# Kernel tuning notes

Hardware: AMD Instinct MI355X
Metric: run time of the kernel (lower is better)

The kernel has to match this reference:

```python
import jax, jax.numpy as jnp
import numpy as np
from jax.ops import segment_sum, segment_max

N_NODES = 50000
N_EDGES = 800000
N_GRAPHS = 512


def setup_inputs() -> dict:
    key = jax.random.key(0)
    ks = jax.random.split(key, 12)
    s = 0.1
    x = jax.random.normal(ks[0], (N_NODES, 3), dtype=jnp.float32)
    edge_index = jax.random.randint(ks[1], (2, N_EDGES), 0, N_NODES, dtype=jnp.int64)
    batch = jnp.sort(jax.random.randint(ks[2], (N_NODES,), 0, N_GRAPHS, dtype=jnp.int64))
    # GATConv(3, 64, heads=4): W [3, 4*64], att [4,64] each
    W1 = jax.random.normal(ks[3], (3, 256), dtype=jnp.float32) * s
    att_src1 = jax.random.normal(ks[4], (4, 64), dtype=jnp.float32) * s
    att_dst1 = jax.random.normal(ks[5], (4, 64), dtype=jnp.float32) * s
    bias1 = jnp.zeros((256,), dtype=jnp.float32)
    # GATConv(256, 128, heads=1)
    W2 = jax.random.normal(ks[6], (256, 128), dtype=jnp.float32) * s
    att_src2 = jax.random.normal(ks[7], (1, 128), dtype=jnp.float32) * s
    att_dst2 = jax.random.normal(ks[8], (1, 128), dtype=jnp.float32) * s
    bias2 = jnp.zeros((128,), dtype=jnp.float32)
    # Linear(128, 2)
    fcW = jax.random.normal(ks[9], (128, 2), dtype=jnp.float32) * s
    fcb = jnp.zeros((2,), dtype=jnp.float32)
    return {"x": x, "edge_index": edge_index, "batch": batch,
            "W1": W1, "att_src1": att_src1, "att_dst1": att_dst1, "bias1": bias1,
            "W2": W2, "att_src2": att_src2, "att_dst2": att_dst2, "bias2": bias2,
            "fcW": fcW, "fcb": fcb}


def gat_conv(x, src, dst, W, att_src, att_dst, bias):
    """PyG-style GATConv (concat heads). src->dst messages, softmax over dst."""
    N = x.shape[0]
    H, C = att_src.shape
    h = (x @ W).reshape(N, H, C)                      # [N,H,C]
    a_src = jnp.einsum('nhc,hc->nh', h, att_src)      # [N,H]
    a_dst = jnp.einsum('nhc,hc->nh', h, att_dst)      # [N,H]
    e = jax.nn.leaky_relu(a_src[src] + a_dst[dst], 0.2)  # [E,H]
    # segment softmax over incoming edges of each dst node
    emax = segment_max(e, dst, num_segments=N)        # [N,H]
    ee = jnp.exp(e - emax[dst])
    denom = segment_sum(ee, dst, num_segments=N)      # [N,H]
    alpha = ee / (denom[dst] + 1e-16)                 # [E,H]
    out = segment_sum(alpha[:, :, None] * h[src], dst, num_segments=N)  # [N,H,C]
    return out.reshape(N, H * C) + bias


def reference(x, edge_index, batch, W1, att_src1, att_dst1, bias1,
              W2, att_src2, att_dst2, bias2, fcW, fcb):
    N = x.shape[0]
    loops = jnp.arange(N, dtype=edge_index.dtype)
    src = jnp.concatenate([edge_index[0], loops])     # add self-loops (PyG default)
    dst = jnp.concatenate([edge_index[1], loops])
    h = jax.nn.relu(gat_conv(x, src, dst, W1, att_src1, att_dst1, bias1))
    h = jax.nn.relu(gat_conv(h, src, dst, W2, att_src2, att_dst2, bias2))
    # global mean pool per graph
    sums = segment_sum(h, batch, num_segments=N_GRAPHS)                # [G,128]
    counts = segment_sum(jnp.ones((N, 1), h.dtype), batch, num_segments=N_GRAPHS)
    pooled = sums / jnp.maximum(counts, 1.0)
    return pooled @ fcW + fcb                          # [G,2]
```

## Files before the change

### kernel.cpp

```cpp
#include <hip/hip_runtime.h>
#include <hip/hip_bf16.h>

#define NN 50000
#define NE 800000
#define NG 512
#define NCHUNK 196
#define NROWPAD 50048
#define CAP 64

#define NBUK 196
#define BCAP 5120
#define BSTRIDE 16
#define LBCAP 32

#define SCAT_BLKS 782
#define A1P_BLKS 196
#define W2B_BLKS 128
#define BND_BLKS 3
#define FRONT_GRID (SCAT_BLKS + A1P_BLKS + W2B_BLKS + BND_BLKS)

typedef __attribute__((ext_vector_type(8))) short bf16x8;
typedef __attribute__((ext_vector_type(4))) float f32x4;

static __device__ __forceinline__ float lrelu(float x) { return x > 0.f ? x : 0.2f * x; }

static __device__ __forceinline__ ushort f2b(float f) {
    __hip_bfloat16 b = __float2bfloat16(f);
    return *(ushort*)&b;
}
static __device__ __forceinline__ float b2f(ushort u) {
    union { unsigned int i; float f; } v; v.i = ((unsigned int)u) << 16; return v.f;
}

__global__ __launch_bounds__(256) void k_front(
        const int* __restrict__ ei, int* __restrict__ bcnt, unsigned int* __restrict__ bstore,
        const float* __restrict__ x, const float* __restrict__ W1,
        const float* __restrict__ attS1, const float* __restrict__ attD1,
        float* __restrict__ xa1, float* __restrict__ a1d,
        const float* __restrict__ W2, ushort* __restrict__ wtb,
        const int* __restrict__ batch, int* __restrict__ bounds) {
    int b = blockIdx.x, tid = threadIdx.x;
    if (b < SCAT_BLKS) {
        __shared__ unsigned int lrec[LBCAP * NBUK];
        __shared__ int lcnt[NBUK];
        for (int i = tid; i < NBUK; i += 256) lcnt[i] = 0;
        __syncthreads();
        int t = b * 256 + tid;
        int base4 = t * 4;
        if (base4 < NE) {
            int4 sv = *(const int4*)(ei + base4);
            int4 dv = *(const int4*)(ei + NE + base4);
            int d, s, bin, p;
            d = dv.x; s = sv.x; bin = d >> 8;
            p = atomicAdd(&lcnt[bin], 1);
            lrec[p * NBUK + bin] = ((unsigned int)s << 8) | (unsigned int)(d & 255);
            d = dv.y; s = sv.y; bin = d >> 8;
            p = atomicAdd(&lcnt[bin], 1);
            lrec[p * NBUK + bin] = ((unsigned int)s << 8) | (unsigned int)(d & 255);
            d = dv.z; s = sv.z; bin = d >> 8;
            p = atomicAdd(&lcnt[bin], 1);
            lrec[p * NBUK + bin] = ((unsigned int)s << 8) | (unsigned int)(d & 255);
            d = dv.w; s = sv.w; bin = d >> 8;
            p = atomicAdd(&lcnt[bin], 1);
            lrec[p * NBUK + bin] = ((unsigned int)s << 8) | (unsigned int)(d & 255);
        }
        __syncthreads();
        if (tid < NBUK) {
            int c = lcnt[tid];
            if (c) {
                int base = atomicAdd(&bcnt[tid * BSTRIDE], c);
                unsigned int* dst = bstore + (size_t)tid * BCAP + base;
                for (int q = 0; q < c; q++) dst[q] = lrec[q * NBUK + tid];
            }
        }
    } else if (b < SCAT_BLKS + A1P_BLKS) {
        __shared__ float wsd[24];
        if (tid < 24) {
            int sel = tid / 12, r = tid % 12;
            int i = r >> 2, h = r & 3;
            const float* att = sel ? attD1 : attS1;
            float s = 0.f;
            for (int c = 0; c < 64; c++) s += W1[i * 256 + h * 64 + c] * att[h * 64 + c];
            wsd[tid] = s;
        }
        __syncthreads();
        int n = (b - SCAT_BLKS) * 256 + tid;
        if (n >= NN) return;
        float x0 = x[n * 3], x1 = x[n * 3 + 1], x2 = x[n * 3 + 2];
        float4 r0, r1, dd;
        r0.x = x0; r0.y = x1; r0.z = x2;
        r0.w = x0 * wsd[0] + x1 * wsd[4] + x2 * wsd[8];
        r1.x = x0 * wsd[1] + x1 * wsd[5] + x2 * wsd[9];
        r1.y = x0 * wsd[2] + x1 * wsd[6] + x2 * wsd[10];
        r1.z = x0 * wsd[3] + x1 * wsd[7] + x2 * wsd[11];
        r1.w = 0.f;
        dd.x = x0 * wsd[12] + x1 * wsd[16] + x2 * wsd[20];
        dd.y = x0 * wsd[13] + x1 * wsd[17] + x2 * wsd[21];
        dd.z = x0 * wsd[14] + x1 * wsd[18] + x2 * wsd[22];
        dd.w = x0 * wsd[15] + x1 * wsd[19] + x2 * wsd[23];
        *(float4*)(xa1 + n * 8) = r0;
        *(float4*)(xa1 + n * 8 + 4) = r1;
        *(float4*)(a1d + n * 4) = dd;
    } else if (b < SCAT_BLKS + A1P_BLKS + W2B_BLKS) {
        int i = (b - SCAT_BLKS - A1P_BLKS) * 256 + tid;
        int k = i >> 7, c = i & 127;
        wtb[c * 256 + k] = f2b(W2[i]);
    } else {
        int g = (b - SCAT_BLKS - A1P_BLKS - W2B_BLKS) * 256 + tid;
        if (g > NG) return;
        int lo = 0, hi = NN;
        while (lo < hi) { int mid = (lo + hi) >> 1; if (batch[mid] < g) lo = mid + 1; else hi = mid; }
        bounds[g] = lo;
    }
}

__global__ __launch_bounds__(256) void k_csr(const int* __restrict__ bcnt,
                                             const unsigned int* __restrict__ bstore,
                                             ushort* __restrict__ csr, int* __restrict__ cnt) {
    __shared__ int cur[256];
    int b = blockIdx.x, tid = threadIdx.x;
    cur[tid] = 0;
    __syncthreads();
    int nb = bcnt[b * BSTRIDE];
    const unsigned int* bp = bstore + (size_t)b * BCAP;
    for (int i = tid; i < nb; i += 256) {
        unsigned int r = bp[i];
        int dlow = r & 255;
        int src = r >> 8;
        int pos = atomicAdd(&cur[dlow], 1);
        csr[(((size_t)b << 8) + dlow) * CAP + pos] = (ushort)src;
    }
    __syncthreads();
    int node = (b << 8) + tid;
    if (node < NN) {
        int c = cur[tid];
        csr[(size_t)node * CAP + c] = (ushort)node;
        cnt[node] = c + 1;
    }
}

__global__ void k_l1_aggr2(const float* __restrict__ xa1, const float* __restrict__ a1d,
                           const int* __restrict__ cnt, const ushort* __restrict__ csr,
                           float* __restrict__ xb) {
    int t = blockIdx.x * 256 + threadIdx.x;
    if (t >= NN * 4) return;
    int n = t >> 2, h = t & 3;
    float adm = a1d[t];
    int dg = cnt[n];
    const ushort* cp = csr + (size_t)n * CAP;
    float a0 = 0.f, a1 = 0.f, a2 = 0.f, l = 0.f;
    int j = 0;
    for (; j + 4 <= dg; j += 4) {
        ushort4 ss = *(const ushort4*)(cp + j);
        int s0 = ss.x, s1 = ss.y, s2 = ss.z, s3 = ss.w;
        float4 r0 = *(const float4*)(xa1 + s0 * 8);
        float4 r1 = *(const float4*)(xa1 + s1 * 8);
        float4 r2 = *(const float4*)(xa1 + s2 * 8);
        float4 r3 = *(const float4*)(xa1 + s3 * 8);
        float g0 = xa1[s0 * 8 + 3 + h];
        float g1 = xa1[s1 * 8 + 3 + h];
        float g2 = xa1[s2 * 8 + 3 + h];
        float g3 = xa1[s3 * 8 + 3 + h];
        float p0 = __expf(lrelu(g0 + adm));
        float p1 = __expf(lrelu(g1 + adm));
        float p2 = __expf(lrelu(g2 + adm));
        float p3 = __expf(lrelu(g3 + adm));
        a0 = fmaf(p0, r0.x, fmaf(p1, r1.x, fmaf(p2, r2.x, fmaf(p3, r3.x, a0))));
        a1 = fmaf(p0, r0.y, fmaf(p1, r1.y, fmaf(p2, r2.y, fmaf(p3, r3.y, a1))));
        a2 = fmaf(p0, r0.z, fmaf(p1, r1.z, fmaf(p2, r2.z, fmaf(p3, r3.z, a2))));
        l += (p0 + p1) + (p2 + p3);
    }
    for (; j < dg; j++) {
        int s = cp[j];
        float4 r = *(const float4*)(xa1 + s * 8);
        float p = __expf(lrelu(xa1[s * 8 + 3 + h] + adm));
        a0 = fmaf(p, r.x, a0);
        a1 = fmaf(p, r.y, a1);
        a2 = fmaf(p, r.z, a2);
        l += p;
    }
    float inv = 1.f / (l + 1e-16f);
    xb[n * 12 + h * 3 + 0] = a0 * inv;
    xb[n * 12 + h * 3 + 1] = a1 * inv;
    xb[n * 12 + h * 3 + 2] = a2 * inv;
}

__global__ __launch_bounds__(64) void k_gemm_mfma(
        const float* __restrict__ xb, const float* __restrict__ W1g,
        const float* __restrict__ b1g, const ushort* __restrict__ wtb,
        const float* __restrict__ attS2, const float* __restrict__ attD2,
        ushort* __restrict__ h2b, float* __restrict__ a2s, float* __restrict__ a2d) {
    __shared__ float W1s[768];
    __shared__ float b1s[256];
    int lane = threadIdx.x;
    int R = blockIdx.x * 32;
    if (R >= NN) return;
    for (int q = lane; q < 768; q += 64) W1s[q] = W1g[q];
    for (int q = lane; q < 256; q += 64) b1s[q] = b1g[q];
    __syncthreads();
    int row16 = lane & 15, kg = lane >> 4;

    float xr[2][12];
#pragma unroll
    for (int t = 0; t < 2; t++) {
        int row = R + t * 16 + row16;
        if (row < NN) {
            *(float4*)(&xr[t][0]) = *(const float4*)(xb + row * 12);
            *(float4*)(&xr[t][4]) = *(const float4*)(xb + row * 12 + 4);
            *(float4*)(&xr[t][8]) = *(const float4*)(xb + row * 12 + 8);
        } else {
#pragma unroll
            for (int q = 0; q < 12; q++) xr[t][q] = 0.f;
        }
    }

    f32x4 acc[2][8];
#pragma unroll
    for (int t = 0; t < 2; t++)
#pragma unroll
        for (int ct = 0; ct < 8; ct++) acc[t][ct] = (f32x4){0.f, 0.f, 0.f, 0.f};

    const ushort* Bb = wtb + (size_t)row16 * 256 + kg * 8;
#pragma unroll
    for (int s = 0; s < 8; s++) {
        int head = s >> 1;
        int c0 = s * 32 + kg * 8;
        bf16x8 a0, a1;
#pragma unroll
        for (int jj = 0; jj < 8; jj++) {
            int c = c0 + jj;
            float w0 = W1s[c], w1 = W1s[256 + c], w2 = W1s[512 + c], bb = b1s[c];
            float v0 = fmaxf(fmaf(xr[0][head * 3], w0, fmaf(xr[0][head * 3 + 1], w1, fmaf(xr[0][head * 3 + 2], w2, bb))), 0.f);
            float v1 = fmaxf(fmaf(xr[1][head * 3], w0, fmaf(xr[1][head * 3 + 1], w1, fmaf(xr[1][head * 3 + 2], w2, bb))), 0.f);
            a0[jj] = (short)f2b(v0);
            a1[jj] = (short)f2b(v1);
        }
#pragma unroll
        for (int ct = 0; ct < 8; ct++) {
            bf16x8 bfr = *(const bf16x8*)(Bb + ct * 16 * 256 + s * 32);
            acc[0][ct] = __builtin_amdgcn_mfma_f32_16x16x32_bf16(a0, bfr, acc[0][ct], 0, 0, 0);
            acc[1][ct] = __builtin_amdgcn_mfma_f32_16x16x32_bf16(a1, bfr, acc[1][ct], 0, 0, 0);
        }
    }

    float s2v[8], d2v[8];
#pragma unroll
    for (int ct = 0; ct < 8; ct++) {
        s2v[ct] = attS2[ct * 16 + row16];
        d2v[ct] = attD2[ct * 16 + row16];
    }
#pragma unroll
    for (int tau = 0; tau < 2; tau++) {
#pragma unroll
        for (int q = 0; q < 4; q++) {
            int row = R + tau * 16 + kg * 4 + q;
            float ps = 0.f, pd = 0.f;
            if (row < NN) {
#pragma unroll
                for (int ct = 0; ct < 8; ct++) {
                    float v = acc[tau][ct][q];
                    h2b[(size_t)row * 128 + ct * 16 + row16] = f2b(v);
                    ps = fmaf(v, s2v[ct], ps);
                    pd = fmaf(v, d2v[ct], pd);
                }
            }
            for (int o = 1; o < 16; o <<= 1) {
                ps += __shfl_xor(ps, o, 64);
                pd += __shfl_xor(pd, o, 64);
            }
            if (row < NN && row16 == 0) { a2s[row] = ps; a2d[row] = pd; }
        }
    }
}

__global__ void k_l2_aggr(const ushort* __restrict__ h2u, const float* __restrict__ a2s,
                          const float* __restrict__ a2d, const int* __restrict__ cnt,
                          const ushort* __restrict__ csr, const float* __restrict__ b2,
                          ushort* __restrict__ out2) {
    int n = blockIdx.x, t = threadIdx.x;
    float adm = a2d[n];
    int dg = cnt[n];
    const ushort* cp = csr + (size_t)n * CAP;
    float accx = 0.f, accy = 0.f, l = 0.f;
    int j = 0;
    for (; j + 8 <= dg; j += 8) {
        ushort4 sA = *(const ushort4*)(cp + j);
        ushort4 sB = *(const ushort4*)(cp + j + 4);
        int s0 = sA.x, s1 = sA.y, s2 = sA.z, s3 = sA.w;
        int s4 = sB.x, s5 = sB.y, s6 = sB.z, s7 = sB.w;
        float e0 = a2s[s0], e1 = a2s[s1], e2 = a2s[s2], e3 = a2s[s3];
        float e4 = a2s[s4], e5 = a2s[s5], e6 = a2s[s6], e7 = a2s[s7];
        ushort2 u0 = *(const ushort2*)(h2u + (size_t)s0 * 128 + t * 2);
        ushort2 u1 = *(const ushort2*)(h2u + (size_t)s1 * 128 + t * 2);
        ushort2 u2 = *(const ushort2*)(h2u + (size_t)s2 * 128 + t * 2);
        ushort2 u3 = *(const ushort2*)(h2u + (size_t)s3 * 128 + t * 2);
        ushort2 u4 = *(const ushort2*)(h2u + (size_t)s4 * 128 + t * 2);
        ushort2 u5 = *(const ushort2*)(h2u + (size_t)s5 * 128 + t * 2);
        ushort2 u6 = *(const ushort2*)(h2u + (size_t)s6 * 128 + t * 2);
        ushort2 u7 = *(const ushort2*)(h2u + (size_t)s7 * 128 + t * 2);
        float p0 = __expf(lrelu(e0 + adm)), p1 = __expf(lrelu(e1 + adm));
        float p2 = __expf(lrelu(e2 + adm)), p3 = __expf(lrelu(e3 + adm));
        float p4 = __expf(lrelu(e4 + adm)), p5 = __expf(lrelu(e5 + adm));
        float p6 = __expf(lrelu(e6 + adm)), p7 = __expf(lrelu(e7 + adm));
        accx = fmaf(p0, b2f(u0.x), fmaf(p1, b2f(u1.x), fmaf(p2, b2f(u2.x), fmaf(p3, b2f(u3.x), accx))));
        accx = fmaf(p4, b2f(u4.x), fmaf(p5, b2f(u5.x), fmaf(p6, b2f(u6.x), fmaf(p7, b2f(u7.x), accx))));
        accy = fmaf(p0, b2f(u0.y), fmaf(p1, b2f(u1.y), fmaf(p2, b2f(u2.y), fmaf(p3, b2f(u3.y), accy))));
        accy = fmaf(p4, b2f(u4.y), fmaf(p5, b2f(u5.y), fmaf(p6, b2f(u6.y), fmaf(p7, b2f(u7.y), accy))));
        l += (p0 + p1) + (p2 + p3) + (p4 + p5) + (p6 + p7);
    }
    for (; j < dg; j++) {
        int s = cp[j];
        float p = __expf(lrelu(a2s[s] + adm));
        ushort2 u = *(const ushort2*)(h2u + (size_t)s * 128 + t * 2);
        accx = fmaf(p, b2f(u.x), accx);
        accy = fmaf(p, b2f(u.y), accy);
        l += p;
    }
    float inv = 1.f / (l + 1e-16f);
    int c = t * 2;
    ushort2 o;
    o.x = f2b(fmaxf(accx * inv + b2[c], 0.f));
    o.y = f2b(fmaxf(accy * inv + b2[c + 1], 0.f));
    *(ushort2*)(out2 + n * 128 + c) = o;
}

__global__ void k_pool_fc(const ushort* __restrict__ out2, const int* __restrict__ bounds,
                          const float* __restrict__ fcW, const float* __restrict__ fcb,
                          float* __restrict__ out) {
    int g = blockIdx.x, t = threadIdx.x;
    int s = bounds[g], e = bounds[g + 1];
    float s0 = 0.f, s1 = 0.f, s2 = 0.f, s3 = 0.f;
    int n = s;
    for (; n + 4 <= e; n += 4) {
        s0 += b2f(out2[n * 128 + t]);
        s1 += b2f(out2[(n + 1) * 128 + t]);
        s2 += b2f(out2[(n + 2) * 128 + t]);
        s3 += b2f(out2[(n + 3) * 128 + t]);
    }
    for (; n < e; n++) s0 += b2f(out2[n * 128 + t]);
    float sum = (s0 + s1) + (s2 + s3);
    float cnt = (float)(e - s);
    float pooled = sum / fmaxf(cnt, 1.f);
    float p0 = pooled * fcW[t * 2 + 0];
    float p1 = pooled * fcW[t * 2 + 1];
    for (int o = 32; o; o >>= 1) {
        p0 += __shfl_down(p0, o, 64);
        p1 += __shfl_down(p1, o, 64);
    }
    __shared__ float l0[2], l1[2];
    if ((t & 63) == 0) { l0[t >> 6] = p0; l1[t >> 6] = p1; }
    __syncthreads();
    if (t == 0) {
        out[g * 2 + 0] = l0[0] + l0[1] + fcb[0];
        out[g * 2 + 1] = l1[0] + l1[1] + fcb[1];
    }
}

extern "C" void kernel_launch(void* const* d_in, const int* in_sizes, int n_in,
                              void* d_out, int out_size, void* d_ws, size_t ws_size,
                              hipStream_t stream) {
    (void)in_sizes; (void)n_in; (void)out_size; (void)ws_size;
    const float* x     = (const float*)d_in[0];
    const int*   ei    = (const int*)d_in[1];
    const int*   batch = (const int*)d_in[2];
    const float* W1    = (const float*)d_in[3];
    const float* attS1 = (const float*)d_in[4];
    const float* attD1 = (const float*)d_in[5];
    const float* b1    = (const float*)d_in[6];
    const float* W2    = (const float*)d_in[7];
    const float* attS2 = (const float*)d_in[8];
    const float* attD2 = (const float*)d_in[9];
    const float* b2    = (const float*)d_in[10];
    const float* fcW   = (const float*)d_in[11];
    const float* fcb   = (const float*)d_in[12];
    float* out = (float*)d_out;

    char* ws = (char*)d_ws;
    size_t off = 0;
    auto alloc = [&](size_t bytes) -> char* {
        char* p = ws + off;
        off = (off + bytes + 255) & ~(size_t)255;
        return p;
    };
    float*  xa1  = (float*)alloc((size_t)NN * 8 * 4);
    float*  a1d  = (float*)alloc((size_t)NN * 4 * 4);
    float*  xb   = (float*)alloc((size_t)NN * 12 * 4);
    int*    cnt  = (int*)alloc((size_t)NN * 4);
    ushort* csr  = (ushort*)alloc((size_t)NN * CAP * 2);
    int*    bcnt = (int*)alloc((size_t)NBUK * BSTRIDE * 4);
    unsigned int* bstore = (unsigned int*)alloc((size_t)NBUK * BCAP * 4);
    ushort* wtb  = (ushort*)alloc((size_t)128 * 256 * 2);
    ushort* h2b  = (ushort*)alloc((size_t)NN * 128 * 2);
    float*  a2s  = (float*)alloc((size_t)NN * 4);
    float*  a2d  = (float*)alloc((size_t)NN * 4);
    int*    bounds = (int*)alloc((size_t)(NG + 1) * 4);
    ushort* out2 = (ushort*)alloc((size_t)NN * 128 * 2);

    hipMemsetAsync(bcnt, 0, (size_t)NBUK * BSTRIDE * 4, stream);
    k_front<<<FRONT_GRID, 256, 0, stream>>>(ei, bcnt, bstore, x, W1, attS1, attD1,
                                            xa1, a1d, W2, wtb, batch, bounds);
    k_csr<<<NBUK, 256, 0, stream>>>(bcnt, bstore, csr, cnt);
    k_l1_aggr2<<<(NN * 4 + 255) / 256, 256, 0, stream>>>(xa1, a1d, cnt, csr, xb);
    k_gemm_mfma<<<(NROWPAD / 32), 64, 0, stream>>>(xb, W1, b1, wtb, attS2, attD2, h2b, a2s, a2d);
    k_l2_aggr<<<NN, 64, 0, stream>>>(h2b, a2s, a2d, cnt, csr, b2, out2);
    k_pool_fc<<<NG, 128, 0, stream>>>(out2, bounds, fcW, fcb, out);
}
```

Before: 125.3 us.

## Fuse mean-pool and FC into layer-2 aggregation via per-node atomics

Each layer-2 node now projects its ReLU output through fcW right away, scales it by the inverse graph size, and atomically adds the two logits into the output. The output is initialized to fcb in the front kernel. This removes the bf16 out2 buffer write/read and the separate pool kernel launch, and packs four nodes per 256-thread block. In exchange it adds 50k float atomics onto 1024 addresses, contention per graph, and a nondeterministic summation order.

```diff
diff --git a/kernel.cpp b/kernel.cpp
--- a/kernel.cpp
+++ b/kernel.cpp
@@ -38,7 +38,8 @@
         const float* __restrict__ attS1, const float* __restrict__ attD1,
         float* __restrict__ xa1, float* __restrict__ a1d,
         const float* __restrict__ W2, ushort* __restrict__ wtb,
-        const int* __restrict__ batch, int* __restrict__ bounds) {
+        const int* __restrict__ batch, int* __restrict__ bounds,
+        const float* __restrict__ fcb, float* __restrict__ out) {
     int b = blockIdx.x, tid = threadIdx.x;
     if (b < SCAT_BLKS) {
         __shared__ unsigned int lrec[LBCAP * NBUK];
@@ -106,7 +107,11 @@
         int k = i >> 7, c = i & 127;
         wtb[c * 256 + k] = f2b(W2[i]);
     } else {
-        int g = (b - SCAT_BLKS - A1P_BLKS - W2B_BLKS) * 256 + tid;
+        int bb = b - SCAT_BLKS - A1P_BLKS - W2B_BLKS;
+        if (bb == 0) {
+            for (int i = tid; i < NG * 2; i += 256) out[i] = fcb[i & 1];
+        }
+        int g = bb * 256 + tid;
         if (g > NG) return;
         int lo = 0, hi = NN;
         while (lo < hi) { int mid = (lo + hi) >> 1; if (batch[mid] < g) lo = mid + 1; else hi = mid; }
@@ -273,11 +278,15 @@
     }
 }
 
-__global__ void k_l2_aggr(const ushort* __restrict__ h2u, const float* __restrict__ a2s,
-                          const float* __restrict__ a2d, const int* __restrict__ cnt,
-                          const ushort* __restrict__ csr, const float* __restrict__ b2,
-                          ushort* __restrict__ out2) {
-    int n = blockIdx.x, t = threadIdx.x;
+__global__ __launch_bounds__(256) void k_l2_aggr(
+        const ushort* __restrict__ h2u, const float* __restrict__ a2s,
+        const float* __restrict__ a2d, const int* __restrict__ cnt,
+        const ushort* __restrict__ csr, const float* __restrict__ b2,
+        const int* __restrict__ batch, const int* __restrict__ bounds,
+        const float* __restrict__ fcW, float* __restrict__ out) {
+    int n = blockIdx.x * 4 + (threadIdx.x >> 6);
+    int t = threadIdx.x & 63;
+    if (n >= NN) return;
     float adm = a2d[n];
     int dg = cnt[n];
     const ushort* cp = csr + (size_t)n * CAP;
@@ -318,41 +327,19 @@
     }
     float inv = 1.f / (l + 1e-16f);
     int c = t * 2;
-    ushort2 o;
-    o.x = f2b(fmaxf(accx * inv + b2[c], 0.f));
-    o.y = f2b(fmaxf(accy * inv + b2[c + 1], 0.f));
-    *(ushort2*)(out2 + n * 128 + c) = o;
-}
-
-__global__ void k_pool_fc(const ushort* __restrict__ out2, const int* __restrict__ bounds,
-                          const float* __restrict__ fcW, const float* __restrict__ fcb,
-                          float* __restrict__ out) {
-    int g = blockIdx.x, t = threadIdx.x;
-    int s = bounds[g], e = bounds[g + 1];
-    float s0 = 0.f, s1 = 0.f, s2 = 0.f, s3 = 0.f;
-    int n = s;
-    for (; n + 4 <= e; n += 4) {
-        s0 += b2f(out2[n * 128 + t]);
-        s1 += b2f(out2[(n + 1) * 128 + t]);
-        s2 += b2f(out2[(n + 2) * 128 + t]);
-        s3 += b2f(out2[(n + 3) * 128 + t]);
-    }
-    for (; n < e; n++) s0 += b2f(out2[n * 128 + t]);
-    float sum = (s0 + s1) + (s2 + s3);
-    float cnt = (float)(e - s);
-    float pooled = sum / fmaxf(cnt, 1.f);
-    float p0 = pooled * fcW[t * 2 + 0];
-    float p1 = pooled * fcW[t * 2 + 1];
+    float ox = fmaxf(accx * inv + b2[c], 0.f);
+    float oy = fmaxf(accy * inv + b2[c + 1], 0.f);
+    float p0 = ox * fcW[c * 2] + oy * fcW[(c + 1) * 2];
+    float p1 = ox * fcW[c * 2 + 1] + oy * fcW[(c + 1) * 2 + 1];
     for (int o = 32; o; o >>= 1) {
         p0 += __shfl_down(p0, o, 64);
         p1 += __shfl_down(p1, o, 64);
     }
-    __shared__ float l0[2], l1[2];
-    if ((t & 63) == 0) { l0[t >> 6] = p0; l1[t >> 6] = p1; }
-    __syncthreads();
     if (t == 0) {
-        out[g * 2 + 0] = l0[0] + l0[1] + fcb[0];
-        out[g * 2 + 1] = l1[0] + l1[1] + fcb[1];
+        int g = batch[n];
+        float ic = 1.f / fmaxf((float)(bounds[g + 1] - bounds[g]), 1.f);
+        atomicAdd(out + g * 2, p0 * ic);
+        atomicAdd(out + g * 2 + 1, p1 * ic);
     }
 }
 
@@ -394,14 +381,13 @@
     float*  a2s  = (float*)alloc((size_t)NN * 4);
     float*  a2d  = (float*)alloc((size_t)NN * 4);
     int*    bounds = (int*)alloc((size_t)(NG + 1) * 4);
-    ushort* out2 = (ushort*)alloc((size_t)NN * 128 * 2);
 
     hipMemsetAsync(bcnt, 0, (size_t)NBUK * BSTRIDE * 4, stream);
     k_front<<<FRONT_GRID, 256, 0, stream>>>(ei, bcnt, bstore, x, W1, attS1, attD1,
-                                            xa1, a1d, W2, wtb, batch, bounds);
+                                            xa1, a1d, W2, wtb, batch, bounds, fcb, out);
     k_csr<<<NBUK, 256, 0, stream>>>(bcnt, bstore, csr, cnt);
     k_l1_aggr2<<<(NN * 4 + 255) / 256, 256, 0, stream>>>(xa1, a1d, cnt, csr, xb);
     k_gemm_mfma<<<(NROWPAD / 32), 64, 0, stream>>>(xb, W1, b1, wtb, attS2, attD2, h2b, a2s, a2d);
-    k_l2_aggr<<<NN, 64, 0, stream>>>(h2b, a2s, a2d, cnt, csr, b2, out2);
-    k_pool_fc<<<NG, 128, 0, stream>>>(out2, bounds, fcW, fcb, out);
-}
+    k_l2_aggr<<<(NN + 3) / 4, 256, 0, stream>>>(h2b, a2s, a2d, cnt, csr, b2,
+                                                batch, bounds, fcW, out);
+}
```

Measured after the change: 201.5 us. 1.61x slower.
